# Performance work log

Hardware: AMD Instinct MI355X
Metric: run time of the kernel (lower is better)

Reference implementation:

```python
import jax, jax.numpy as jnp
import numpy as np

SX = 512; SY = 512; C = 3; NK = 10; R = 10
DT = 0.2; DD = 5; SIGMA = 0.65; THETA_A = 1.0; NPOW = 2


def setup_inputs() -> dict:
    rng = np.random.RandomState(0)
    r = rng.uniform(0.3, 1.0, NK).astype(np.float32)
    m = rng.uniform(0.05, 0.5, NK).astype(np.float32)
    s = rng.uniform(0.01, 0.18, NK).astype(np.float32)
    h = rng.uniform(0.2, 1.0, NK).astype(np.float32)
    a = rng.uniform(0.0, 1.0, (NK, 3)).astype(np.float32)
    w = rng.uniform(0.01, 0.5, (NK, 3)).astype(np.float32)
    b = rng.uniform(0.0, 1.0, (NK, 3)).astype(np.float32)
    # compute_kernel(): radial distance grid, ring sigmoid * sum-of-bumps ker_f, normalized
    mid = SX // 2
    x = np.linspace(-mid, mid, 2 * mid, dtype=np.float32)
    X, Y = np.meshgrid(x, x, indexing='ij')
    dist = np.sqrt(X ** 2 + Y ** 2)
    D = dist[:, :, None] / ((R + 15.0) * r)                      # (SX, SY, NK)
    ring = 1.0 / (1.0 + np.exp((D - 1.0) * 10.0))                # sigmoid(-(D-1)*10)
    bumps = (b * np.exp(-((D[..., None] - a) ** 2) / w)).sum(-1)  # ker_f(D, a, w, b)
    K = (ring * bumps).astype(np.float32)
    nK_ker = K / K.sum(axis=(0, 1), keepdims=True)               # (SX, SY, NK)
    # kernel -> source channel, and kernel -> target channel one-hot (c1 as matrix)
    c0 = np.array([0, 0, 0, 1, 1, 1, 2, 2, 2, 0], dtype=np.int32)
    tgt = np.array([0, 1, 2, 0, 1, 2, 0, 1, 2, 0], dtype=np.int32)
    c1_mat = np.zeros((NK, C), dtype=np.int32)
    c1_mat[np.arange(NK), tgt] = 1
    key = jax.random.key(0)
    A = jax.random.uniform(key, (SX, SY, C), dtype=jnp.float32)  # scale_init_state = 1
    return {"A": A, "nK_ker": jnp.asarray(nK_ker), "m": jnp.asarray(m),
            "s": jnp.asarray(s), "h": jnp.asarray(h),
            "c0": jnp.asarray(c0), "c1_mat": jnp.asarray(c1_mat)}


def _sobel(A):
    """A: (SX, SY, Cc) -> (SX, SY, 2, Cc), circular (toroidal) boundary."""
    def grad_ax(ax):
        sm_ax = 1 - ax
        sm = jnp.roll(A, 1, sm_ax) + 2.0 * A + jnp.roll(A, -1, sm_ax)  # [1,2,1] smoothing
        return (jnp.roll(sm, -1, ax) - jnp.roll(sm, 1, ax)) / 8.0       # central diff
    return jnp.stack([grad_ax(0), grad_ax(1)], axis=2)


def _flowlenia_step(A, nK_ker, m, s, h, c0, c1_mat):
    # FFT Lenia convolution
    fA = jnp.fft.fft2(A, axes=(0, 1))                              # (SX, SY, C) complex
    fK = jnp.fft.fft2(jnp.fft.fftshift(nK_ker, axes=(0, 1)), axes=(0, 1))
    U = jnp.real(jnp.fft.ifft2(fK * fA[:, :, c0], axes=(0, 1)))    # (SX, SY, NK)
    # growth * h, then gather-sum kernels into target channels (c1)
    U = (2.0 * jnp.exp(-((U - m) ** 2) / (2.0 * s ** 2)) - 1.0) * h
    U = jnp.einsum('xyk,kc->xyc', U, c1_mat.astype(U.dtype))       # (SX, SY, C)
    # flow field
    nabla_U = _sobel(U)                                            # (SX, SY, 2, C)
    nabla_A = _sobel(A.sum(-1, keepdims=True))                     # (SX, SY, 2, 1)
    alpha = jnp.clip((A[:, :, None, :] / THETA_A) ** NPOW, 0.0, 1.0)
    F = nabla_U * (1.0 - alpha) - nabla_A * alpha                  # (SX, SY, 2, C)
    # reintegration tracking (mass-conserving advection over (2*DD+1)^2 shifts)
    xs = jnp.arange(SX, dtype=A.dtype)
    ys = jnp.arange(SY, dtype=A.dtype)
    X, Y = jnp.meshgrid(xs, ys, indexing='ij')
    pos = jnp.stack([X, Y], axis=-1) + 0.5                         # (SX, SY, 2) cell centers
    ma = DD - SIGMA                                                # max flow magnitude
    mu = pos[..., None] + DT * jnp.clip(F, -ma, ma)                # (SX, SY, 2, C)
    shifts = jnp.array([(dx, dy) for dx in range(-DD, DD + 1)
                        for dy in range(-DD, DD + 1)], dtype=jnp.int32)
    clip_hi = min(1.0, 2.0 * SIGMA)
    inv_norm = 1.0 / (4.0 * SIGMA ** 2)

    def body(acc, sh):
        dx, dy = sh[0], sh[1]
        rA = jnp.roll(jnp.roll(A, dx, 0), dy, 1)
        rmu = jnp.roll(jnp.roll(mu, dx, 0), dy, 1)
        sz = 0.5 - jnp.abs(pos[..., None] - rmu) + SIGMA
        area = jnp.prod(jnp.clip(sz, 0.0, clip_hi), axis=2) * inv_norm  # (SX, SY, C)
        return acc + rA * area, None

    nA, _ = jax.lax.scan(body, jnp.zeros_like(A), shifts)
    return nA


def reference(A, nK_ker, m, s, h, c0, c1_mat):
    return _flowlenia_step(A, nK_ker, m, s, h, c0, c1_mat)
```

## Files before the change

kernel.cpp:

```cpp
#include <hip/hip_runtime.h>
#include <math.h>

#define NF 512
#define NF2 (NF * NF)
#define RPB 4
#define PI_F 3.14159265358979323846f

typedef float2 Row[NF];

__device__ inline Row* fft512(Row* SA, Row* SB, const float2* W, int tid, float dsign) {
    int r = tid >> 6, tr = tid & 63;
    Row* S = SA; Row* D = SB;
    int m = 1;
    for (int st = 0; st < 9; ++st) {
        __syncthreads();
#pragma unroll
        for (int q = 0; q < 4; ++q) {
            int b = tr + (q << 6);
            int widx = b & ~(m - 1);
            float2 c0 = S[r][b];
            float2 c1 = S[r][b + 256];
            float2 w = W[widx];
            float wre = w.x, wim = dsign * w.y;
            float sx = c0.x + c1.x, sy = c0.y + c1.y;
            float tx = c0.x - c1.x, ty = c0.y - c1.y;
            int o = b + widx;
            D[r][o] = make_float2(sx, sy);
            D[r][o + m] = make_float2(tx * wre - ty * wim, tx * wim + ty * wre);
        }
        Row* t = S; S = D; D = t;
        m <<= 1;
    }
    __syncthreads();
    return S;
}

#define FFT_SHARED                                     \
    __shared__ float2 SA[RPB][NF];                     \
    __shared__ float2 SB[RPB][NF];                     \
    __shared__ float2 W[256];                          \
    int tid = threadIdx.x;                             \
    {                                                  \
        float sn, cs;                                  \
        sincosf((PI_F / 256.0f) * (float)tid, &sn, &cs); \
        W[tid] = make_float2(cs, sn);                  \
    }

__device__ inline float2 unpack_field(const float2* __restrict__ Z, int plane, int slot,
                                      int ky, int kx) {
    const float2* P = Z + (size_t)plane * NF2;
    float2 zr = P[(ky << 9) + kx];
    float2 zm = P[(((NF - ky) & (NF - 1)) << 9) + ((NF - kx) & (NF - 1))];
    if (slot == 0)
        return make_float2(0.5f * (zr.x + zm.x), 0.5f * (zr.y - zm.y));
    else
        return make_float2(0.5f * (zr.y + zm.y), 0.5f * (zm.x - zr.x));
}

__global__ __launch_bounds__(256) void k_fwd_p1(const float* __restrict__ A,
                                                const float* __restrict__ K,
                                                float2* __restrict__ Z) {
    FFT_SHARED
    int p = blockIdx.y;
    const float* bre; int sre, cre;
    const float* bim; int sim, cim;
    switch (p) {
        case 0: bre = A; sre = 3; cre = 0; bim = A; sim = 3; cim = 1; break;
        case 1: bre = A; sre = 3; cre = 2; bim = K; sim = 10; cim = 0; break;
        case 2: bre = K; sre = 10; cre = 1; bim = K; sim = 10; cim = 2; break;
        case 3: bre = K; sre = 10; cre = 3; bim = K; sim = 10; cim = 4; break;
        case 4: bre = K; sre = 10; cre = 5; bim = K; sim = 10; cim = 6; break;
        case 5: bre = K; sre = 10; cre = 7; bim = K; sim = 10; cim = 8; break;
        default: bre = K; sre = 10; cre = 9; bim = nullptr; sim = 0; cim = 0; break;
    }
    int x0 = blockIdx.x * RPB;
    for (int i = tid; i < RPB * NF; i += 256) {
        int r = i >> 9, y = i & (NF - 1);
        int idx = ((x0 + r) << 9) + y;
        float vr = bre[idx * sre + cre];
        float vi = bim ? bim[idx * sim + cim] : 0.0f;
        SA[r][y] = make_float2(vr, vi);
    }
    Row* R = fft512(SA, SB, W, tid, -1.0f);
    for (int i = tid; i < RPB * NF; i += 256) {
        int r = i & (RPB - 1), ky = i >> 2;
        Z[(size_t)((p << 9) + ky) * NF + x0 + r] = R[r][ky];
    }
}

__global__ __launch_bounds__(256) void k_fft_rows(float2* __restrict__ data, float dsign) {
    FFT_SHARED
    int R0 = blockIdx.x * RPB;
    for (int i = tid; i < RPB * NF; i += 256) {
        int r = i >> 9, x = i & (NF - 1);
        SA[r][x] = data[(size_t)(R0 + r) * NF + x];
    }
    Row* R = fft512(SA, SB, W, tid, dsign);
    for (int i = tid; i < RPB * NF; i += 256) {
        int r = i >> 9, x = i & (NF - 1);
        data[(size_t)(R0 + r) * NF + x] = R[r][x];
    }
}

__global__ __launch_bounds__(256) void k_mulinv_p1(const float2* __restrict__ Z,
                                                   const int* __restrict__ c0,
                                                   float2* __restrict__ tmp) {
    FFT_SHARED
    int j = blockIdx.y;
    int k1 = 2 * j, k2 = 2 * j + 1;
    int pK1 = (k1 == 0) ? 1 : 2 + ((k1 - 1) >> 1);
    int sK1 = (k1 == 0) ? 1 : ((k1 - 1) & 1);
    int pK2 = 2 + ((k2 - 1) >> 1);
    int sK2 = (k2 - 1) & 1;
    int cA1 = c0[k1], cA2 = c0[k2];
    int pA1 = cA1 >> 1, sA1 = cA1 & 1;
    int pA2 = cA2 >> 1, sA2 = cA2 & 1;
    bool sameA = (cA1 == cA2);

    int ky0 = blockIdx.x * RPB;
    for (int i = tid; i < RPB * NF; i += 256) {
        int r = i >> 9, kx = i & (NF - 1);
        int ky = ky0 + r;
        float2 fk1 = unpack_field(Z, pK1, sK1, ky, kx);
        float2 fk2 = unpack_field(Z, pK2, sK2, ky, kx);
        float2 fa1 = unpack_field(Z, pA1, sA1, ky, kx);
        float2 fa2 = sameA ? fa1 : unpack_field(Z, pA2, sA2, ky, kx);
        float t1x = fk1.x * fa1.x - fk1.y * fa1.y;
        float t1y = fk1.x * fa1.y + fk1.y * fa1.x;
        float t2x = fk2.x * fa2.x - fk2.y * fa2.y;
        float t2y = fk2.x * fa2.y + fk2.y * fa2.x;
        float sgn = ((kx + ky) & 1) ? -1.0f : 1.0f;
        SA[r][kx] = make_float2((t1x - t2y) * sgn, (t1y + t2x) * sgn);
    }
    Row* R = fft512(SA, SB, W, tid, +1.0f);
    for (int i = tid; i < RPB * NF; i += 256) {
        int r = i & (RPB - 1), x = i >> 2;
        tmp[(size_t)(j * NF + x) * NF + ky0 + r] = R[r][x];
    }
}

__global__ __launch_bounds__(256) void k_inv_p2g(const float2* __restrict__ tmp,
                                                 const float* __restrict__ mm,
                                                 const float* __restrict__ ss,
                                                 const float* __restrict__ hh,
                                                 float* __restrict__ G) {
    FFT_SHARED
    int j = blockIdx.y;
    int k1 = 2 * j, k2 = 2 * j + 1;
    int x0 = blockIdx.x * RPB;
    for (int i = tid; i < RPB * NF; i += 256) {
        int r = i >> 9, ky = i & (NF - 1);
        SA[r][ky] = tmp[(size_t)(j * NF + x0 + r) * NF + ky];
    }
    Row* R = fft512(SA, SB, W, tid, +1.0f);
    float m1 = mm[k1], s1 = ss[k1], h1 = hh[k1];
    float m2 = mm[k2], s2 = ss[k2], h2 = hh[k2];
    float i2s1 = 1.0f / (2.0f * s1 * s1);
    float i2s2 = 1.0f / (2.0f * s2 * s2);
    const float scale = 1.0f / ((float)NF * (float)NF);
    for (int i = tid; i < RPB * NF; i += 256) {
        int r = i >> 9, y = i & (NF - 1);
        float2 v = R[r][y];
        float u1 = v.x * scale, u2 = v.y * scale;
        float d1 = u1 - m1, d2 = u2 - m2;
        size_t base = (size_t)(x0 + r) * NF + y;
        G[(size_t)k1 * NF2 + base] = (2.0f * expf(-d1 * d1 * i2s1) - 1.0f) * h1;
        G[(size_t)k2 * NF2 + base] = (2.0f * expf(-d2 * d2 * i2s2) - 1.0f) * h2;
    }
}

__global__ __launch_bounds__(256) void k_combine(const float* __restrict__ G,
                                                 const int* __restrict__ c1,
                                                 const float* __restrict__ A,
                                                 float* __restrict__ Up,
                                                 float* __restrict__ As) {
    int id = blockIdx.x * 256 + threadIdx.x;
    float a0 = 0.f, a1 = 0.f, a2 = 0.f;
#pragma unroll
    for (int k = 0; k < 10; ++k) {
        float g = G[k * NF2 + id];
        a0 += g * (float)c1[k * 3 + 0];
        a1 += g * (float)c1[k * 3 + 1];
        a2 += g * (float)c1[k * 3 + 2];
    }
    Up[id] = a0;
    Up[NF2 + id] = a1;
    Up[2 * NF2 + id] = a2;
    As[id] = A[id * 3 + 0] + A[id * 3 + 1] + A[id * 3 + 2];
}

__global__ __launch_bounds__(256) void k_flow(const float* __restrict__ Up,
                                              const float* __restrict__ As,
                                              const float* __restrict__ A,
                                              float* __restrict__ mu) {
    int id = blockIdx.x * 256 + threadIdx.x;
    int x = id >> 9, y = id & (NF - 1);
    int xm = (x - 1) & (NF - 1), xp = (x + 1) & (NF - 1);
    int ym = (y - 1) & (NF - 1), yp = (y + 1) & (NF - 1);

    auto grad = [&](const float* f, float& gx, float& gy) {
        float fmm = f[xm * NF + ym], fm0 = f[xm * NF + y], fmp = f[xm * NF + yp];
        float f0m = f[x * NF + ym], f0p = f[x * NF + yp];
        float fpm = f[xp * NF + ym], fp0 = f[xp * NF + y], fpp = f[xp * NF + yp];
        gx = (fpm + 2.0f * fp0 + fpp - fmm - 2.0f * fm0 - fmp) * 0.125f;
        gy = (fmp + 2.0f * f0p + fpp - fmm - 2.0f * f0m - fpm) * 0.125f;
    };

    float gax, gay;
    grad(As, gax, gay);
    float px = (float)x + 0.5f, py = (float)y + 0.5f;
#pragma unroll
    for (int c = 0; c < 3; ++c) {
        float gux, guy;
        grad(Up + c * NF2, gux, guy);
        float a = A[id * 3 + c];
        float al = fminf(a * a, 1.0f);
        float Fx = gux * (1.0f - al) - gax * al;
        float Fy = guy * (1.0f - al) - gay * al;
        Fx = fminf(fmaxf(Fx, -4.35f), 4.35f);
        Fy = fminf(fmaxf(Fy, -4.35f), 4.35f);
        mu[c * NF2 + id] = px + 0.2f * Fx;
        mu[(3 + c) * NF2 + id] = py + 0.2f * Fy;
    }
}

__global__ __launch_bounds__(256) void k_reint(const float* __restrict__ A,
                                               const float* __restrict__ mu,
                                               float* __restrict__ out) {
    __shared__ float sA[3][36 * 36];
    __shared__ float sM[6][36 * 36];
    int tid = threadIdx.x;
    int x0 = blockIdx.x * 32, y0 = blockIdx.y * 32;
    for (int i = tid; i < 36 * 36; i += 256) {
        int lx = i / 36, ly = i - lx * 36;
        int xg = (x0 - 2 + lx) & (NF - 1);
        int yg = (y0 - 2 + ly) & (NF - 1);
        int gid = xg * NF + yg;
        sA[0][i] = A[gid * 3 + 0];
        sA[1][i] = A[gid * 3 + 1];
        sA[2][i] = A[gid * 3 + 2];
#pragma unroll
        for (int p = 0; p < 6; ++p) sM[p][i] = mu[p * NF2 + gid];
    }
    __syncthreads();

    const float INV_NORM = (float)(1.0 / (4.0 * 0.65 * 0.65));
    int cy = tid & 31, cx0 = tid >> 5;
    for (int sidx = 0; sidx < 4; ++sidx) {
        int cx = cx0 + 8 * sidx;
        int x = x0 + cx, y = y0 + cy;
        float px = (float)x + 0.5f, py = (float)y + 0.5f;
        float acc0 = 0.f, acc1 = 0.f, acc2 = 0.f;
#pragma unroll
        for (int dx = 0; dx < 5; ++dx)
#pragma unroll
            for (int dy = 0; dy < 5; ++dy) {
                int li = (cx + dx) * 36 + (cy + dy);
#pragma unroll
                for (int c = 0; c < 3; ++c) {
                    float mux = sM[c][li], muy = sM[3 + c][li];
                    float szx = 0.5f - fabsf(px - mux) + 0.65f;
                    float szy = 0.5f - fabsf(py - muy) + 0.65f;
                    szx = fminf(fmaxf(szx, 0.0f), 1.0f);
                    szy = fminf(fmaxf(szy, 0.0f), 1.0f);
                    float area = szx * szy * INV_NORM;
                    float v = sA[c][li] * area;
                    if (c == 0) acc0 += v;
                    else if (c == 1) acc1 += v;
                    else acc2 += v;
                }
            }
        int gid = x * NF + y;
        out[gid * 3 + 0] = acc0;
        out[gid * 3 + 1] = acc1;
        out[gid * 3 + 2] = acc2;
    }
}

extern "C" void kernel_launch(void* const* d_in, const int* in_sizes, int n_in,
                              void* d_out, int out_size, void* d_ws, size_t ws_size,
                              hipStream_t stream) {
    (void)in_sizes; (void)n_in; (void)out_size; (void)ws_size;
    const float* A  = (const float*)d_in[0];
    const float* nK = (const float*)d_in[1];
    const float* m  = (const float*)d_in[2];
    const float* s  = (const float*)d_in[3];
    const float* h  = (const float*)d_in[4];
    const int*   c0 = (const int*)d_in[5];
    const int*   c1 = (const int*)d_in[6];
    float* out = (float*)d_out;

    char* ws = (char*)d_ws;
    float2* Z   = (float2*)ws;
    float2* tmp = (float2*)(ws + 14680064);
    float*  G   = (float*)ws;
    float*  Up  = (float*)(ws + 10485760);
    float*  As  = (float*)(ws + 13631488);
    float*  mu  = (float*)(ws + 14680064);

    dim3 blk(256);
    k_fwd_p1<<<dim3(NF / RPB, 7), blk, 0, stream>>>(A, nK, Z);
    k_fft_rows<<<dim3(7 * NF / RPB), blk, 0, stream>>>(Z, -1.0f);
    k_mulinv_p1<<<dim3(NF / RPB, 5), blk, 0, stream>>>(Z, c0, tmp);
    k_inv_p2g<<<dim3(NF / RPB, 5),   blk, 0, stream>>>(tmp, m, s, h, G);
    k_combine<<<dim3(NF2 / 256), blk, 0, stream>>>(G, c1, A, Up, As);
    k_flow<<<dim3(NF2 / 256),    blk, 0, stream>>>(Up, As, A, mu);
    k_reint<<<dim3(16, 16),      blk, 0, stream>>>(A, mu, out);
}
```

Baseline: 155.8 us.

## Replace radix-2 shared-memory FFT with register radix-8 three-pass FFT

Replaces the 9-stage radix-2 FFT, which bounces through shared memory with a barrier per stage, with a radix-8 decomposition. Each thread holds 8 points in registers and does three radix-8 passes, with only two shared-memory exchanges. The shared rows are padded (LPAD) to avoid bank conflicts, and inputs are loaded directly into registers. This cuts barriers and LDS traffic across all FFT kernels, at the cost of more registers per thread and twiddles computed by repeated complex multiplication, which adds some rounding error.

```diff
diff --git a/kernel.cpp b/kernel.cpp
--- a/kernel.cpp
+++ b/kernel.cpp
@@ -4,46 +4,84 @@
 #define NF 512
 #define NF2 (NF * NF)
 #define RPB 4
+#define ROWLEN 580
 #define PI_F 3.14159265358979323846f
 
-typedef float2 Row[NF];
-
-__device__ inline Row* fft512(Row* SA, Row* SB, const float2* W, int tid, float dsign) {
-    int r = tid >> 6, tr = tid & 63;
-    Row* S = SA; Row* D = SB;
-    int m = 1;
-    for (int st = 0; st < 9; ++st) {
-        __syncthreads();
-#pragma unroll
-        for (int q = 0; q < 4; ++q) {
-            int b = tr + (q << 6);
-            int widx = b & ~(m - 1);
-            float2 c0 = S[r][b];
-            float2 c1 = S[r][b + 256];
-            float2 w = W[widx];
-            float wre = w.x, wim = dsign * w.y;
-            float sx = c0.x + c1.x, sy = c0.y + c1.y;
-            float tx = c0.x - c1.x, ty = c0.y - c1.y;
-            int o = b + widx;
-            D[r][o] = make_float2(sx, sy);
-            D[r][o + m] = make_float2(tx * wre - ty * wim, tx * wim + ty * wre);
-        }
-        Row* t = S; S = D; D = t;
-        m <<= 1;
-    }
-    __syncthreads();
-    return S;
-}
-
-#define FFT_SHARED                                     \
-    __shared__ float2 SA[RPB][NF];                     \
-    __shared__ float2 SB[RPB][NF];                     \
-    __shared__ float2 W[256];                          \
-    int tid = threadIdx.x;                             \
-    {                                                  \
-        float sn, cs;                                  \
-        sincosf((PI_F / 256.0f) * (float)tid, &sn, &cs); \
-        W[tid] = make_float2(cs, sn);                  \
+#define LPAD(q) ((q) + ((q) >> 3))
+
+__device__ inline float2 cadd(float2 a, float2 b) { return make_float2(a.x + b.x, a.y + b.y); }
+__device__ inline float2 csub(float2 a, float2 b) { return make_float2(a.x - b.x, a.y - b.y); }
+__device__ inline float2 cmul(float2 a, float2 b) {
+    return make_float2(a.x * b.x - a.y * b.y, a.x * b.y + a.y * b.x);
+}
+
+__device__ inline void fft8(float2 x[8], float dsign) {
+    const float s = 0.70710678118654752440f;
+    float2 a0 = cadd(x[0], x[4]), a1 = cadd(x[1], x[5]);
+    float2 a2 = cadd(x[2], x[6]), a3 = cadd(x[3], x[7]);
+    float2 b0 = csub(x[0], x[4]), b1 = csub(x[1], x[5]);
+    float2 b2 = csub(x[2], x[6]), b3 = csub(x[3], x[7]);
+    b1 = cmul(b1, make_float2(s, dsign * s));
+    b2 = make_float2(-dsign * b2.y, dsign * b2.x);
+    b3 = cmul(b3, make_float2(-s, dsign * s));
+    float2 c0 = cadd(a0, a2), c1 = cadd(a1, a3);
+    float2 c2 = csub(a0, a2), c3 = csub(a1, a3);
+    c3 = make_float2(-dsign * c3.y, dsign * c3.x);
+    float2 d0 = cadd(b0, b2), d1 = cadd(b1, b3);
+    float2 d2 = csub(b0, b2), d3 = csub(b1, b3);
+    d3 = make_float2(-dsign * d3.y, dsign * d3.x);
+    x[0] = cadd(c0, c1); x[4] = csub(c0, c1);
+    x[2] = cadd(c2, c3); x[6] = csub(c2, c3);
+    x[1] = cadd(d0, d1); x[5] = csub(d0, d1);
+    x[3] = cadd(d2, d3); x[7] = csub(d2, d3);
+}
+
+__device__ inline void twiddle8(float2 x[8], float2 wb) {
+    float2 tw = wb;
+    x[1] = cmul(x[1], tw); tw = cmul(tw, wb);
+    x[2] = cmul(x[2], tw); tw = cmul(tw, wb);
+    x[3] = cmul(x[3], tw); tw = cmul(tw, wb);
+    x[4] = cmul(x[4], tw); tw = cmul(tw, wb);
+    x[5] = cmul(x[5], tw); tw = cmul(tw, wb);
+    x[6] = cmul(x[6], tw); tw = cmul(tw, wb);
+    x[7] = cmul(x[7], tw);
+}
+
+__device__ inline void fft512_regs(float2 x[8], int b, float2* bufA, float2* bufB,
+                                   const float2* Wt, float dsign) {
+    fft8(x, dsign);
+    float2 wb0 = make_float2(Wt[b].x, dsign * Wt[b].y);
+    twiddle8(x, wb0);
+#pragma unroll
+    for (int p = 0; p < 8; ++p) bufA[9 * b + p] = x[p];
+    __syncthreads();
+#pragma unroll
+    for (int j = 0; j < 8; ++j) x[j] = bufA[LPAD(b + 64 * j)];
+    fft8(x, dsign);
+    int u = b >> 3, v = b & 7;
+    float2 wb1 = make_float2(Wt[b & ~7].x, dsign * Wt[b & ~7].y);
+    twiddle8(x, wb1);
+    int base = u * 64 + v;
+#pragma unroll
+    for (int p = 0; p < 8; ++p) bufB[LPAD(base + 8 * p)] = x[p];
+    __syncthreads();
+#pragma unroll
+    for (int j = 0; j < 8; ++j) x[j] = bufB[LPAD(b + 64 * j)];
+    fft8(x, dsign);
+}
+
+#define FFT_PRE                                                    \
+    __shared__ float2 SHA[RPB][ROWLEN];                            \
+    __shared__ float2 SHB[RPB][ROWLEN];                            \
+    __shared__ float2 Wt[512];                                     \
+    int tid = threadIdx.x;                                         \
+    int rr_ = tid >> 6, bb_ = tid & 63;                            \
+    {                                                              \
+        float sn, cs;                                              \
+        sincosf((PI_F / 256.0f) * (float)tid, &sn, &cs);           \
+        Wt[tid] = make_float2(cs, sn);                             \
+        sincosf((PI_F / 256.0f) * (float)(tid + 256), &sn, &cs);   \
+        Wt[tid + 256] = make_float2(cs, sn);                       \
     }
 
 __device__ inline float2 unpack_field(const float2* __restrict__ Z, int plane, int slot,
@@ -60,11 +98,11 @@
 __global__ __launch_bounds__(256) void k_fwd_p1(const float* __restrict__ A,
                                                 const float* __restrict__ K,
                                                 float2* __restrict__ Z) {
-    FFT_SHARED
-    int p = blockIdx.y;
+    FFT_PRE
+    int pl = blockIdx.y;
     const float* bre; int sre, cre;
     const float* bim; int sim, cim;
-    switch (p) {
+    switch (pl) {
         case 0: bre = A; sre = 3; cre = 0; bim = A; sim = 3; cim = 1; break;
         case 1: bre = A; sre = 3; cre = 2; bim = K; sim = 10; cim = 0; break;
         case 2: bre = K; sre = 10; cre = 1; bim = K; sim = 10; cim = 2; break;
@@ -74,40 +112,50 @@
         default: bre = K; sre = 10; cre = 9; bim = nullptr; sim = 0; cim = 0; break;
     }
     int x0 = blockIdx.x * RPB;
-    for (int i = tid; i < RPB * NF; i += 256) {
-        int r = i >> 9, y = i & (NF - 1);
-        int idx = ((x0 + r) << 9) + y;
+    int row = x0 + rr_;
+    float2 x[8];
+#pragma unroll
+    for (int j = 0; j < 8; ++j) {
+        int idx = (row << 9) + bb_ + 64 * j;
         float vr = bre[idx * sre + cre];
         float vi = bim ? bim[idx * sim + cim] : 0.0f;
-        SA[r][y] = make_float2(vr, vi);
-    }
-    Row* R = fft512(SA, SB, W, tid, -1.0f);
+        x[j] = make_float2(vr, vi);
+    }
+    __syncthreads();
+    fft512_regs(x, bb_, &SHA[rr_][0], &SHB[rr_][0], Wt, -1.0f);
+#pragma unroll
+    for (int p2 = 0; p2 < 8; ++p2) SHA[rr_][LPAD(64 * p2 + bb_)] = x[p2];
+    __syncthreads();
     for (int i = tid; i < RPB * NF; i += 256) {
-        int r = i & (RPB - 1), ky = i >> 2;
-        Z[(size_t)((p << 9) + ky) * NF + x0 + r] = R[r][ky];
+        int r2 = i & (RPB - 1), ky = i >> 2;
+        Z[(size_t)((pl << 9) + ky) * NF + x0 + r2] = SHA[r2][LPAD(ky)];
     }
 }
 
 __global__ __launch_bounds__(256) void k_fft_rows(float2* __restrict__ data, float dsign) {
-    FFT_SHARED
+    FFT_PRE
     int R0 = blockIdx.x * RPB;
+    size_t rowbase = (size_t)(R0 + rr_) * NF;
+    float2 x[8];
+#pragma unroll
+    for (int j = 0; j < 8; ++j) x[j] = data[rowbase + bb_ + 64 * j];
+    __syncthreads();
+    fft512_regs(x, bb_, &SHA[rr_][0], &SHB[rr_][0], Wt, dsign);
+#pragma unroll
+    for (int p2 = 0; p2 < 8; ++p2) SHA[rr_][LPAD(64 * p2 + bb_)] = x[p2];
+    __syncthreads();
     for (int i = tid; i < RPB * NF; i += 256) {
-        int r = i >> 9, x = i & (NF - 1);
-        SA[r][x] = data[(size_t)(R0 + r) * NF + x];
-    }
-    Row* R = fft512(SA, SB, W, tid, dsign);
-    for (int i = tid; i < RPB * NF; i += 256) {
-        int r = i >> 9, x = i & (NF - 1);
-        data[(size_t)(R0 + r) * NF + x] = R[r][x];
+        int r2 = i >> 9, xx = i & (NF - 1);
+        data[(size_t)(R0 + r2) * NF + xx] = SHA[r2][LPAD(xx)];
     }
 }
 
 __global__ __launch_bounds__(256) void k_mulinv_p1(const float2* __restrict__ Z,
                                                    const int* __restrict__ c0,
                                                    float2* __restrict__ tmp) {
-    FFT_SHARED
-    int j = blockIdx.y;
-    int k1 = 2 * j, k2 = 2 * j + 1;
+    FFT_PRE
+    int jp = blockIdx.y;
+    int k1 = 2 * jp, k2 = 2 * jp + 1;
     int pK1 = (k1 == 0) ? 1 : 2 + ((k1 - 1) >> 1);
     int sK1 = (k1 == 0) ? 1 : ((k1 - 1) & 1);
     int pK2 = 2 + ((k2 - 1) >> 1);
@@ -118,9 +166,11 @@
     bool sameA = (cA1 == cA2);
 
     int ky0 = blockIdx.x * RPB;
-    for (int i = tid; i < RPB * NF; i += 256) {
-        int r = i >> 9, kx = i & (NF - 1);
-        int ky = ky0 + r;
+    int ky = ky0 + rr_;
+    float2 x[8];
+#pragma unroll
+    for (int jj = 0; jj < 8; ++jj) {
+        int kx = bb_ + 64 * jj;
         float2 fk1 = unpack_field(Z, pK1, sK1, ky, kx);
         float2 fk2 = unpack_field(Z, pK2, sK2, ky, kx);
         float2 fa1 = unpack_field(Z, pA1, sA1, ky, kx);
@@ -130,12 +180,16 @@
         float t2x = fk2.x * fa2.x - fk2.y * fa2.y;
         float t2y = fk2.x * fa2.y + fk2.y * fa2.x;
         float sgn = ((kx + ky) & 1) ? -1.0f : 1.0f;
-        SA[r][kx] = make_float2((t1x - t2y) * sgn, (t1y + t2x) * sgn);
-    }
-    Row* R = fft512(SA, SB, W, tid, +1.0f);
+        x[jj] = make_float2((t1x - t2y) * sgn, (t1y + t2x) * sgn);
+    }
+    __syncthreads();
+    fft512_regs(x, bb_, &SHA[rr_][0], &SHB[rr_][0], Wt, +1.0f);
+#pragma unroll
+    for (int p2 = 0; p2 < 8; ++p2) SHA[rr_][LPAD(64 * p2 + bb_)] = x[p2];
+    __syncthreads();
     for (int i = tid; i < RPB * NF; i += 256) {
-        int r = i & (RPB - 1), x = i >> 2;
-        tmp[(size_t)(j * NF + x) * NF + ky0 + r] = R[r][x];
+        int r2 = i & (RPB - 1), xx = i >> 2;
+        tmp[(size_t)(jp * NF + xx) * NF + ky0 + r2] = SHA[r2][LPAD(xx)];
     }
 }
 
@@ -144,28 +198,30 @@
                                                  const float* __restrict__ ss,
                                                  const float* __restrict__ hh,
                                                  float* __restrict__ G) {
-    FFT_SHARED
-    int j = blockIdx.y;
-    int k1 = 2 * j, k2 = 2 * j + 1;
+    FFT_PRE
+    int jp = blockIdx.y;
+    int k1 = 2 * jp, k2 = 2 * jp + 1;
     int x0 = blockIdx.x * RPB;
-    for (int i = tid; i < RPB * NF; i += 256) {
-        int r = i >> 9, ky = i & (NF - 1);
-        SA[r][ky] = tmp[(size_t)(j * NF + x0 + r) * NF + ky];
-    }
-    Row* R = fft512(SA, SB, W, tid, +1.0f);
+    int row = x0 + rr_;
+    size_t base = (size_t)(jp * NF + row) * NF;
+    float2 x[8];
+#pragma unroll
+    for (int j2 = 0; j2 < 8; ++j2) x[j2] = tmp[base + bb_ + 64 * j2];
+    __syncthreads();
+    fft512_regs(x, bb_, &SHA[rr_][0], &SHB[rr_][0], Wt, +1.0f);
     float m1 = mm[k1], s1 = ss[k1], h1 = hh[k1];
     float m2 = mm[k2], s2 = ss[k2], h2 = hh[k2];
     float i2s1 = 1.0f / (2.0f * s1 * s1);
     float i2s2 = 1.0f / (2.0f * s2 * s2);
     const float scale = 1.0f / ((float)NF * (float)NF);
-    for (int i = tid; i < RPB * NF; i += 256) {
-        int r = i >> 9, y = i & (NF - 1);
-        float2 v = R[r][y];
-        float u1 = v.x * scale, u2 = v.y * scale;
+#pragma unroll
+    for (int p2 = 0; p2 < 8; ++p2) {
+        int y = 64 * p2 + bb_;
+        float u1 = x[p2].x * scale, u2 = x[p2].y * scale;
         float d1 = u1 - m1, d2 = u2 - m2;
-        size_t base = (size_t)(x0 + r) * NF + y;
-        G[(size_t)k1 * NF2 + base] = (2.0f * expf(-d1 * d1 * i2s1) - 1.0f) * h1;
-        G[(size_t)k2 * NF2 + base] = (2.0f * expf(-d2 * d2 * i2s2) - 1.0f) * h2;
+        size_t o = (size_t)row * NF + y;
+        G[(size_t)k1 * NF2 + o] = (2.0f * expf(-d1 * d1 * i2s1) - 1.0f) * h1;
+        G[(size_t)k2 * NF2 + o] = (2.0f * expf(-d2 * d2 * i2s2) - 1.0f) * h2;
     }
 }
 
```

Measured after the change: 142.5 us. 8.5% less time.
